# Kernel optimization log

Hardware: AMD Instinct MI355X
Metric: run time of the kernel (lower is better)

## Reference

```python
import jax, jax.numpy as jnp
import numpy as np
import math

NUM_STEPS = 100
SIGMA_R, SIGMA_T = 0.05, 0.03
B, HO = 4096, 64

def _alpha_bars(n=NUM_STEPS):
    # squaredcos_cap_v2 schedule (betas_for_alpha_bar), then cumprod of alphas via log-cumsum-exp
    def ab(t):
        return math.cos((t + 0.008) / 1.008 * math.pi / 2) ** 2
    betas = np.array([min(1.0 - ab((i + 1) / n) / ab(i / n), 0.999) for i in range(n)], np.float64)
    return np.exp(np.cumsum(np.log(1.0 - betas))).astype(np.float32)

def _hat(w):
    x, y, z = w[..., 0], w[..., 1], w[..., 2]
    o = jnp.zeros_like(x)
    return jnp.stack([
        jnp.stack([o, -z, y], -1),
        jnp.stack([z, o, -x], -1),
        jnp.stack([-y, x, o], -1)], -2)

def se3_exp(xi):
    # xi: (...,6) = [omega(3), v(3)]  (rotation first, matching sigma_r/sigma_t ordering)
    w, v = xi[..., :3], xi[..., 3:]
    th2 = jnp.sum(w * w, -1)
    small = th2 < 1e-8
    th2s = jnp.where(small, 1.0, th2)
    th = jnp.sqrt(th2s)
    A = jnp.where(small, 1.0 - th2 / 6.0, jnp.sin(th) / th)
    Bc = jnp.where(small, 0.5 - th2 / 24.0, (1.0 - jnp.cos(th)) / th2s)
    Cc = jnp.where(small, 1.0 / 6.0 - th2 / 120.0, (th - jnp.sin(th)) / (th2s * th))
    K = _hat(w)
    K2 = K @ K
    I3 = jnp.eye(3, dtype=xi.dtype)
    R = I3 + A[..., None, None] * K + Bc[..., None, None] * K2
    V = I3 + Bc[..., None, None] * K + Cc[..., None, None] * K2
    t = jnp.einsum('...ij,...j->...i', V, v)
    top = jnp.concatenate([R, t[..., None]], -1)  # (...,3,4)
    bot = jnp.broadcast_to(jnp.array([0., 0., 0., 1.], xi.dtype), top.shape[:-2] + (1, 4))
    return jnp.concatenate([top, bot], -2)

def se3_log(H):
    # H: (...,4,4) -> (...,6) = [omega, v]
    R = H[..., :3, :3]
    t = H[..., :3, 3]
    vee = 0.5 * jnp.stack([R[..., 2, 1] - R[..., 1, 2],
                           R[..., 0, 2] - R[..., 2, 0],
                           R[..., 1, 0] - R[..., 0, 1]], -1)  # sin(theta)*axis
    cos_t = jnp.clip(0.5 * (jnp.trace(R, axis1=-2, axis2=-1) - 1.0), -1.0, 1.0)
    s2 = jnp.sum(vee * vee, -1)  # sin(theta)^2
    small = s2 < 1e-12
    sin_s = jnp.sqrt(jnp.where(small, 1.0, s2))
    th = jnp.arctan2(sin_s, cos_t)  # valid in the non-small branch
    fac = jnp.where(small, 1.0 + s2 / 6.0, th / sin_s)  # theta / sin(theta)
    w = fac[..., None] * vee
    # V^{-1} = I - K/2 + D * K^2 ; D -> 1/12 as theta -> 0
    one_m_cos = jnp.where(small, 1.0, 1.0 - cos_t)
    th2s = jnp.where(small, 1.0, th * th)
    D = jnp.where(small, 1.0 / 12.0 + s2 / 720.0,
                  (1.0 - th * sin_s / (2.0 * one_m_cos)) / th2s)
    K = _hat(w)
    I3 = jnp.eye(3, dtype=H.dtype)
    Vinv = I3 - 0.5 * K + D[..., None, None] * (K @ K)
    v = jnp.einsum('...ij,...j->...i', Vinv, t)
    return jnp.concatenate([w, v], -1)

def _add_noise(twist, noise, alpha_bars, timesteps):
    original = se3_exp(twist)                 # (B,Ho,4,4) valid SE(3) samples
    ab = alpha_bars[timesteps][:, None, None]  # (B,1,1)
    H_inv = jnp.linalg.inv(original)           # H_T @ inv(orig) with H_T = I
    xi = se3_log(H_inv)
    H_t = se3_exp((1.0 - jnp.sqrt(ab)) * xi) @ original
    scale = jnp.concatenate([jnp.full((3,), SIGMA_R, jnp.float32),
                             jnp.full((3,), SIGMA_T, jnp.float32)])
    n = jnp.sqrt(1.0 - ab) * scale * noise
    H_noise = se3_exp(n)
    return H_noise @ H_t, H_noise

def setup_inputs() -> dict:
    key = jax.random.key(0)
    k1, k2, k3 = jax.random.split(key, 3)
    twist = 0.5 * jax.random.normal(k1, (B, HO, 6), jnp.float32)  # keeps angle << pi
    noise = jax.random.normal(k2, (B, HO, 6), jnp.float32)
    timesteps = jax.random.randint(k3, (B,), 0, NUM_STEPS)
    return {"twist": twist, "noise": noise,
            "alpha_bars": jnp.asarray(_alpha_bars()), "timesteps": timesteps}

def reference(twist, noise, alpha_bars, timesteps):
    return _add_noise(twist, noise, alpha_bars, timesteps)
```

## Files before the change

kernel.cpp:

```cpp
#include <hip/hip_runtime.h>
#include <math.h>

constexpr int B_DIM = 4096;
constexpr int HO_DIM = 64;
constexpr int NTOT = B_DIM * HO_DIM;
constexpr int MPB  = 256;
constexpr int NBLK = NTOT / MPB;
constexpr float SIGMA_R = 0.05f;
constexpr float SIGMA_T = 0.03f;

typedef float f4 __attribute__((ext_vector_type(4)));
typedef float f2 __attribute__((ext_vector_type(2)));

__device__ __forceinline__ void exp_se3(float x, float y, float z,
                                        float vx, float vy, float vz,
                                        float R[9], float t[3]) {
    float th2 = x*x + y*y + z*z;
    bool small = th2 < 1e-8f;
    float th2s = small ? 1.0f : th2;
    float th = __builtin_amdgcn_sqrtf(th2s);
    float s = __sinf(th);
    float c = __cosf(th);
    float rth  = __builtin_amdgcn_rcpf(th);
    float rth2 = rth * rth;
    float A  = small ? (1.0f - th2 * (1.0f/6.0f))        : (s * rth);
    float Bc = small ? (0.5f - th2 * (1.0f/24.0f))       : ((1.0f - c) * rth2);
    float Cc = small ? (1.0f/6.0f - th2 * (1.0f/120.0f)) : ((th - s) * rth2 * rth);
    R[0] = 1.0f + Bc*(x*x - th2);
    R[1] = -A*z + Bc*x*y;
    R[2] =  A*y + Bc*x*z;
    R[3] =  A*z + Bc*x*y;
    R[4] = 1.0f + Bc*(y*y - th2);
    R[5] = -A*x + Bc*y*z;
    R[6] = -A*y + Bc*x*z;
    R[7] =  A*x + Bc*y*z;
    R[8] = 1.0f + Bc*(z*z - th2);
    float V0 = 1.0f + Cc*(x*x - th2);
    float V1 = -Bc*z + Cc*x*y;
    float V2 =  Bc*y + Cc*x*z;
    float V3 =  Bc*z + Cc*x*y;
    float V4 = 1.0f + Cc*(y*y - th2);
    float V5 = -Bc*x + Cc*y*z;
    float V6 = -Bc*y + Cc*x*z;
    float V7 =  Bc*x + Cc*y*z;
    float V8 = 1.0f + Cc*(z*z - th2);
    t[0] = V0*vx + V1*vy + V2*vz;
    t[1] = V3*vx + V4*vy + V5*vz;
    t[2] = V6*vx + V7*vy + V8*vz;
}

__global__ __launch_bounds__(256) void DiffusionScheduler_kernel(
    const float* __restrict__ twist, const float* __restrict__ noise,
    const float* __restrict__ alpha_bars, const int* __restrict__ timesteps,
    float* __restrict__ out)
{
    __shared__ float lds[12][258];

    int t = threadIdx.x;
    size_t mat = (size_t)blockIdx.x * MPB + t;

    int ts = timesteps[mat >> 6];
    float ab = alpha_bars[ts];
    float sab = __builtin_amdgcn_sqrtf(ab);
    float sq  = __builtin_amdgcn_sqrtf(1.0f - ab);
    float kr = sq * SIGMA_R, kt = sq * SIGMA_T;

    const f2* nz = (const f2*)(noise + 6 * mat);
    f2 n0 = nz[0], n1 = nz[1], n2 = nz[2];
    const f2* tw = (const f2*)(twist + 6 * mat);
    f2 a0 = tw[0], a1 = tw[1], a2 = tw[2];

    float Rn[9], tn[3];
    exp_se3(kr*n0.x, kr*n0.y, kr*n1.x, kt*n1.y, kt*n2.x, kt*n2.y, Rn, tn);

    lds[ 0][t] = Rn[0]; lds[ 1][t] = Rn[1]; lds[ 2][t] = Rn[2]; lds[ 3][t] = tn[0];
    lds[ 4][t] = Rn[3]; lds[ 5][t] = Rn[4]; lds[ 6][t] = Rn[5]; lds[ 7][t] = tn[1];
    lds[ 8][t] = Rn[6]; lds[ 9][t] = Rn[7]; lds[10][t] = Rn[8]; lds[11][t] = tn[2];

    __syncthreads();

    int rr = t & 3;
    int mb = t >> 2;
    f4* o0 = ((f4*)out) + (size_t)blockIdx.x * (MPB * 4);
    f4* o1 = o0 + (size_t)NTOT * 4;

    #pragma unroll
    for (int c = 0; c < 4; ++c) {
        int m = c * 64 + mb;
        f4 v = (rr == 3) ? (f4){0.0f, 0.0f, 0.0f, 1.0f}
                         : (f4){lds[4*rr+0][m], lds[4*rr+1][m], lds[4*rr+2][m], lds[4*rr+3][m]};
        __builtin_nontemporal_store(v, &o1[c * 256 + t]);
    }

    float Rt[9], tt[3];
    exp_se3(sab*a0.x, sab*a0.y, sab*a1.x, sab*a1.y, sab*a2.x, sab*a2.y, Rt, tt);

    float R0[9], t0[3];
    #pragma unroll
    for (int r = 0; r < 3; ++r) {
        #pragma unroll
        for (int cdx = 0; cdx < 3; ++cdx) {
            R0[3*r+cdx] = Rn[3*r+0]*Rt[0+cdx] + Rn[3*r+1]*Rt[3+cdx] + Rn[3*r+2]*Rt[6+cdx];
        }
    }
    t0[0] = Rn[0]*tt[0]+Rn[1]*tt[1]+Rn[2]*tt[2] + tn[0];
    t0[1] = Rn[3]*tt[0]+Rn[4]*tt[1]+Rn[5]*tt[2] + tn[1];
    t0[2] = Rn[6]*tt[0]+Rn[7]*tt[1]+Rn[8]*tt[2] + tn[2];

    __syncthreads();

    lds[ 0][t] = R0[0]; lds[ 1][t] = R0[1]; lds[ 2][t] = R0[2]; lds[ 3][t] = t0[0];
    lds[ 4][t] = R0[3]; lds[ 5][t] = R0[4]; lds[ 6][t] = R0[5]; lds[ 7][t] = t0[1];
    lds[ 8][t] = R0[6]; lds[ 9][t] = R0[7]; lds[10][t] = R0[8]; lds[11][t] = t0[2];

    __syncthreads();

    #pragma unroll
    for (int c = 0; c < 4; ++c) {
        int m = c * 64 + mb;
        f4 v = (rr == 3) ? (f4){0.0f, 0.0f, 0.0f, 1.0f}
                         : (f4){lds[4*rr+0][m], lds[4*rr+1][m], lds[4*rr+2][m], lds[4*rr+3][m]};
        __builtin_nontemporal_store(v, &o0[c * 256 + t]);
    }
}

extern "C" void kernel_launch(void* const* d_in, const int* in_sizes, int n_in,
                              void* d_out, int out_size, void* d_ws, size_t ws_size,
                              hipStream_t stream) {
    const float* twist       = (const float*)d_in[0];
    const float* noise       = (const float*)d_in[1];
    const float* alpha_bars  = (const float*)d_in[2];
    const int*   timesteps   = (const int*)d_in[3];
    float* out = (float*)d_out;

    dim3 block(256);
    dim3 grid(NBLK);
    hipLaunchKernelGGL(DiffusionScheduler_kernel, grid, block, 0, stream,
                       twist, noise, alpha_bars, timesteps, out);
}
```

Before: 14.04 us.

## Use per-wave f4 LDS staging with wave barriers instead of block syncs

The shared-memory transpose is now done separately by each wavefront. Each wave stages its 64 matrices as padded float4 rows and writes its own contiguous 256-float4 slice of the output. This replaces the block-wide __syncthreads with wave barriers and the scalar LDS accesses with 128-bit ones, and the nontemporal stores become plain stores. It relies on wavefront-64 lockstep semantics for correctness, and the stride-5 float4 padding may still cause some LDS bank conflicts.

```diff
diff --git a/kernel.cpp b/kernel.cpp
--- a/kernel.cpp
+++ b/kernel.cpp
@@ -54,9 +54,11 @@
     const float* __restrict__ alpha_bars, const int* __restrict__ timesteps,
     float* __restrict__ out)
 {
-    __shared__ float lds[12][258];
+    __shared__ f4 lds4[4 * 64 * 5];
 
-    int t = threadIdx.x;
+    int t  = threadIdx.x;
+    int w  = t >> 6;
+    int tl = t & 63;
     size_t mat = (size_t)blockIdx.x * MPB + t;
 
     int ts = timesteps[mat >> 6];
@@ -73,24 +75,26 @@
     float Rn[9], tn[3];
     exp_se3(kr*n0.x, kr*n0.y, kr*n1.x, kt*n1.y, kt*n2.x, kt*n2.y, Rn, tn);
 
-    lds[ 0][t] = Rn[0]; lds[ 1][t] = Rn[1]; lds[ 2][t] = Rn[2]; lds[ 3][t] = tn[0];
-    lds[ 4][t] = Rn[3]; lds[ 5][t] = Rn[4]; lds[ 6][t] = Rn[5]; lds[ 7][t] = tn[1];
-    lds[ 8][t] = Rn[6]; lds[ 9][t] = Rn[7]; lds[10][t] = Rn[8]; lds[11][t] = tn[2];
+    f4* wl = lds4 + w * 320;
+    wl[tl*5+0] = (f4){Rn[0], Rn[1], Rn[2], tn[0]};
+    wl[tl*5+1] = (f4){Rn[3], Rn[4], Rn[5], tn[1]};
+    wl[tl*5+2] = (f4){Rn[6], Rn[7], Rn[8], tn[2]};
 
-    __syncthreads();
+    __builtin_amdgcn_wave_barrier();
 
-    int rr = t & 3;
-    int mb = t >> 2;
-    f4* o0 = ((f4*)out) + (size_t)blockIdx.x * (MPB * 4);
+    int rr = tl & 3;
+    int qq = tl >> 2;
+    f4* o0 = ((f4*)out) + (size_t)blockIdx.x * (MPB * 4) + w * 256;
     f4* o1 = o0 + (size_t)NTOT * 4;
 
     #pragma unroll
     for (int c = 0; c < 4; ++c) {
-        int m = c * 64 + mb;
         f4 v = (rr == 3) ? (f4){0.0f, 0.0f, 0.0f, 1.0f}
-                         : (f4){lds[4*rr+0][m], lds[4*rr+1][m], lds[4*rr+2][m], lds[4*rr+3][m]};
-        __builtin_nontemporal_store(v, &o1[c * 256 + t]);
+                         : wl[(16*c + qq) * 5 + rr];
+        o1[c * 64 + tl] = v;
     }
+
+    __builtin_amdgcn_wave_barrier();
 
     float Rt[9], tt[3];
     exp_se3(sab*a0.x, sab*a0.y, sab*a1.x, sab*a1.y, sab*a2.x, sab*a2.y, Rt, tt);
@@ -107,20 +111,17 @@
     t0[1] = Rn[3]*tt[0]+Rn[4]*tt[1]+Rn[5]*tt[2] + tn[1];
     t0[2] = Rn[6]*tt[0]+Rn[7]*tt[1]+Rn[8]*tt[2] + tn[2];
 
-    __syncthreads();
+    wl[tl*5+0] = (f4){R0[0], R0[1], R0[2], t0[0]};
+    wl[tl*5+1] = (f4){R0[3], R0[4], R0[5], t0[1]};
+    wl[tl*5+2] = (f4){R0[6], R0[7], R0[8], t0[2]};
 
-    lds[ 0][t] = R0[0]; lds[ 1][t] = R0[1]; lds[ 2][t] = R0[2]; lds[ 3][t] = t0[0];
-    lds[ 4][t] = R0[3]; lds[ 5][t] = R0[4]; lds[ 6][t] = R0[5]; lds[ 7][t] = t0[1];
-    lds[ 8][t] = R0[6]; lds[ 9][t] = R0[7]; lds[10][t] = R0[8]; lds[11][t] = t0[2];
-
-    __syncthreads();
+    __builtin_amdgcn_wave_barrier();
 
     #pragma unroll
     for (int c = 0; c < 4; ++c) {
-        int m = c * 64 + mb;
         f4 v = (rr == 3) ? (f4){0.0f, 0.0f, 0.0f, 1.0f}
-                         : (f4){lds[4*rr+0][m], lds[4*rr+1][m], lds[4*rr+2][m], lds[4*rr+3][m]};
-        __builtin_nontemporal_store(v, &o0[c * 256 + t]);
+                         : wl[(16*c + qq) * 5 + rr];
+        o0[c * 64 + tl] = v;
     }
 }
 
```

Result: no change. 14.02 us (-0.1%).
